# Performance work log

Measured on AMD Instinct MI355X. Metric: run time of the kernel, lower is better.

Reference implementation:

```python
import jax, jax.numpy as jnp
import numpy as np

IN, HID, OUT, HEADS = 64, 128, 256, 4
BL, N, E = 4, 2500, 120000
NT = BL * N  # total flattened nodes = 10000
NEG_SLOPE = 0.2  # PyG GATv2Conv default


def setup_inputs() -> dict:
    key = jax.random.key(0)
    ks = jax.random.split(key, 32)
    inp = {}
    inp["x"] = jax.random.normal(ks[0], (BL, N, IN), jnp.float32)
    inp["edge_index"] = jax.random.randint(ks[1], (2, E), 0, NT, jnp.int32)
    inp["edge_weight"] = jax.random.uniform(ks[2], (E, 1), jnp.float32)
    # layers: (fan_in, out_per_head, heads)
    dims = [(IN, HID, HEADS), (HID * HEADS, HID, HEADS), (HID * HEADS, OUT, 1)]
    i = 3
    for l, (fi, fo, h) in enumerate(dims):
        sc = 1.0 / np.sqrt(fi)
        inp[f"Wl{l}"] = jax.random.normal(ks[i], (fi, h * fo), jnp.float32) * sc
        inp[f"bl{l}"] = jax.random.normal(ks[i + 1], (h * fo,), jnp.float32) * 0.01
        inp[f"Wr{l}"] = jax.random.normal(ks[i + 2], (fi, h * fo), jnp.float32) * sc
        inp[f"br{l}"] = jax.random.normal(ks[i + 3], (h * fo,), jnp.float32) * 0.01
        inp[f"We{l}"] = jax.random.normal(ks[i + 4], (1, h * fo), jnp.float32)
        inp[f"att{l}"] = jax.random.normal(ks[i + 5], (h, fo), jnp.float32) / np.sqrt(fo)
        inp[f"bias{l}"] = jax.random.normal(ks[i + 6], (h * fo,), jnp.float32) * 0.01
        i += 7
    return inp


def _gat_layer(x, src, dst, ew, Wl, bl, Wr, br, We, att, bias):
    # x: (NT, F); ew: (E, 1); att: (H, C)
    H, C = att.shape
    n = x.shape[0]
    xl = (x @ Wl + bl).reshape(n, H, C)          # source transform
    xr = (x @ Wr + br).reshape(n, H, C)          # target transform
    xe = (ew @ We).reshape(-1, H, C)             # edge-attr transform (no bias in PyG lin_edge)
    e = jax.nn.leaky_relu(xl[src] + xr[dst] + xe, negative_slope=NEG_SLOPE)  # (E, H, C)
    logits = jnp.einsum('ehc,hc->eh', e, att)    # (E, H)
    # segment softmax over incoming edges of each destination node
    m = jax.lax.stop_gradient(jax.ops.segment_max(logits, dst, num_segments=n))
    m = jnp.where(jnp.isfinite(m), m, 0.0)
    p = jnp.exp(logits - m[dst])
    s = jax.ops.segment_sum(p, dst, num_segments=n)
    alpha = p / (s[dst] + 1e-16)                 # (E, H)
    msg = xl[src] * alpha[:, :, None]            # (E, H, C)
    out = jax.ops.segment_sum(msg, dst, num_segments=n)  # (NT, H, C)
    return out.reshape(n, H * C) + bias


def reference(x, edge_index, edge_weight,
              Wl0, bl0, Wr0, br0, We0, att0, bias0,
              Wl1, bl1, Wr1, br1, We1, att1, bias1,
              Wl2, bl2, Wr2, br2, We2, att2, bias2):
    bl_, n_, f_ = x.shape
    h = x.reshape(bl_ * n_, f_)
    src, dst = edge_index[0], edge_index[1]
    h = jax.nn.elu(_gat_layer(h, src, dst, edge_weight, Wl0, bl0, Wr0, br0, We0, att0, bias0))
    h = jax.nn.elu(_gat_layer(h, src, dst, edge_weight, Wl1, bl1, Wr1, br1, We1, att1, bias1))
    h = _gat_layer(h, src, dst, edge_weight, Wl2, bl2, Wr2, br2, We2, att2, bias2)
    return h.reshape(bl_, n_, -1)
```

## Files before the change

### kernel.cpp

```cpp
#include <hip/hip_runtime.h>
#include <hip/hip_bf16.h>
#include <math.h>

#define NT    10000
#define NE    120000
#define MP    10240

using h8    = __attribute__((ext_vector_type(8))) _Float16;
using h4    = __attribute__((ext_vector_type(4))) _Float16;
using f32x4 = __attribute__((ext_vector_type(4))) float;

struct Args {
    const float* x;
    const int*   src;
    const int*   dst;
    const float* ew;
    const float* W[6];
    const float* bl[3];
    const float* br[3];
    const float* We[3];
    const float* att[3];
    const float* bias[3];
    _Float16* wt[6];
    _Float16* xf;
    _Float16* xl;  _Float16* xr;
    _Float16* af;
    float* out;
    int* rowptr; int* cntcur; int* csr_src; float* csr_w;
};

__global__ void prep_k(Args a) {
    __shared__ float sf[32 * 33];
    const int mat_cum[7] = {0, 32, 64, 320, 576, 704, 832};
    const int mat_K[6]   = {64, 64, 512, 512, 512, 512};
    const int mat_N[6]   = {512, 512, 512, 512, 256, 256};
    int tid = threadIdx.x;
    int tx = tid & 31, ty = tid >> 5;
    for (int w = blockIdx.x; w < 3411; w += gridDim.x) {
        if (w < 79) {
            int i = w * 256 + tid;
            if (i < 2 * NT) a.cntcur[i] = 0;
        } else if (w < 911) {
            int t = w - 79;
            int mm = 0;
            #pragma unroll
            for (int q = 1; q < 6; ++q) if (t >= mat_cum[q]) mm = q;
            int tt = t - mat_cum[mm];
            int K = mat_K[mm], N = mat_N[mm];
            int tiles_k = K >> 5;
            int tk = tt % tiles_k, tn = tt / tiles_k;
            const float* W = a.W[mm];
            _Float16* T = a.wt[mm];
            int bk = tk * 32, bn = tn * 32;
            __syncthreads();
            #pragma unroll
            for (int i = 0; i < 4; ++i)
                sf[(ty * 4 + i) * 33 + tx] =
                    W[(size_t)(bk + ty * 4 + i) * N + bn + tx];
            __syncthreads();
            #pragma unroll
            for (int i = 0; i < 4; ++i) {
                int nn = ty * 4 + i;
                T[(size_t)(bn + nn) * K + bk + tx] = (_Float16)sf[tx * 33 + nn];
            }
        } else {
            int i = (w - 911) * 256 + tid;
            a.xf[i] = (_Float16)a.x[i];
        }
    }
}

__global__ void hist_k(Args a) {
    for (int e = blockIdx.x * 256 + threadIdx.x; e < NE; e += gridDim.x * 256)
        atomicAdd(&a.cntcur[a.dst[e]], 1);
}

__global__ void scan_k(Args a) {
    __shared__ int si[256];
    int tid = threadIdx.x;
    const int PER = 40;
    int base = tid * PER;
    int s = 0;
    for (int i = 0; i < PER; ++i) {
        int idx = base + i;
        if (idx < NT) s += a.cntcur[idx];
    }
    si[tid] = s;
    __syncthreads();
    for (int off = 1; off < 256; off <<= 1) {
        int v = (tid >= off) ? si[tid - off] : 0;
        __syncthreads();
        si[tid] += v;
        __syncthreads();
    }
    int run = (tid == 0) ? 0 : si[tid - 1];
    for (int i = 0; i < PER; ++i) {
        int idx = base + i;
        if (idx < NT) { a.rowptr[idx] = run; run += a.cntcur[idx]; }
        else if (idx == NT) a.rowptr[idx] = run;
    }
}

__global__ void scatter_k(Args a) {
    int* cursor = a.cntcur + NT;
    for (int e = blockIdx.x * 256 + threadIdx.x; e < NE; e += gridDim.x * 256) {
        int d = a.dst[e];
        int pos = atomicAdd(&cursor[d], 1);
        int idx = a.rowptr[d] + pos;
        a.csr_src[idx] = a.src[e];
        a.csr_w[idx]  = a.ew[e];
    }
}

__global__ __launch_bounds__(256, 4) void gemm_k(
    const _Float16* __restrict__ A,
    const _Float16* __restrict__ WlT, const _Float16* __restrict__ WrT,
    const float* __restrict__ biasl, const float* __restrict__ biasr,
    _Float16* __restrict__ outl, _Float16* __restrict__ outr,
    int M, int N, int K)
{
    __shared__ __align__(16) _Float16 sm[2 * 8192];
    _Float16* sA = sm;
    _Float16* sB = sm + 8192;

    int tid = threadIdx.x;
    int wave = tid >> 6, lane = tid & 63;
    int job = blockIdx.x;

    int xcd = job & 7;
    int kk  = job >> 3;
    int r   = kk % 10;
    int byy = kk / 10;
    int bm  = (xcd * 10 + r) * 128;

    int nby = N >> 7;
    bool isR = byy >= nby;
    int bnn = (isR ? byy - nby : byy) << 7;
    const _Float16* Bh = isR ? WrT : WlT;
    const float* bias  = isR ? biasr : biasl;
    _Float16* out      = isR ? outr : outl;

    int lr15 = lane & 15;
    int lk8  = (lane >> 4) * 8;
    int fq = lane >> 4;
    int fc = lane & 15;
    int wm = (wave & 1) << 6;
    int wn = (wave >> 1) << 6;

    f32x4 acc[4][4] = {};

    for (int k0 = 0; k0 < K; k0 += 64) {
        __syncthreads();
        #pragma unroll
        for (int q = 0; q < 8; ++q) {
            int p = wave * 8 + q;
            int bufi = p >> 4;
            int c = p & 15;
            int sub = c >> 3, rg = c & 7;
            const _Float16* g = (bufi == 0) ? A : Bh;
            int rowbase = (bufi == 0) ? bm : bnn;
            _Float16* sb = sm + bufi * 8192 + c * 512;
            const _Float16* gp = g + (size_t)(rowbase + rg * 16 + lr15) * K
                                   + k0 + sub * 32 + lk8;
            __builtin_amdgcn_global_load_lds(
                (const __attribute__((address_space(1))) void*)gp,
                (__attribute__((address_space(3))) void*)sb,
                16, 0, 0);
        }
        __syncthreads();

        #pragma unroll
        for (int sub = 0; sub < 2; ++sub) {
            h8 af[4];
            #pragma unroll
            for (int i = 0; i < 4; ++i) {
                int c = sub * 8 + (wave & 1) * 4 + i;
                af[i] = *(const h8*)(sA + c * 512 + lane * 8);
            }
            #pragma unroll
            for (int j = 0; j < 4; ++j) {
                int c = sub * 8 + (wave >> 1) * 4 + j;
                h8 bf = *(const h8*)(sB + c * 512 + lane * 8);
                #pragma unroll
                for (int i = 0; i < 4; ++i)
                    acc[i][j] = __builtin_amdgcn_mfma_f32_16x16x32_f16(af[i], bf, acc[i][j], 0, 0, 0);
            }
        }
    }

    #pragma unroll
    for (int j = 0; j < 4; ++j) {
        int col = bnn + wn + j * 16 + fc;
        float bv = bias[col];
        #pragma unroll
        for (int i = 0; i < 4; ++i) {
            int row0 = bm + wm + i * 16 + fq * 4;
            #pragma unroll
            for (int reg = 0; reg < 4; ++reg) {
                int row = row0 + reg;
                if (row < M)
                    out[(size_t)row * N + col] = (_Float16)(acc[i][j][reg] + bv);
            }
        }
    }
}

template<int C, int H, bool DO_ELU, bool FP16OUT>
__global__ __launch_bounds__(256) void edge_k(
    const _Float16* __restrict__ xl, const _Float16* __restrict__ xr,
    const int* __restrict__ rowptr, const int* __restrict__ csr_src,
    const float* __restrict__ csr_w,
    const float* __restrict__ We, const float* __restrict__ att,
    const float* __restrict__ bias,
    float* __restrict__ outf, _Float16* __restrict__ outh)
{
    constexpr int CHT = C * H;
    constexpr int VPT = CHT / 64;
    constexpr int G   = 64 / H;

    int node = (blockIdx.x * 256 + threadIdx.x) >> 6;
    int lane = threadIdx.x & 63;
    if (node >= NT) return;
    int c0 = lane * VPT;
    size_t nbase = (size_t)node * CHT + c0;

    float xr_reg[VPT], we_reg[VPT], att_reg[VPT], bias_reg[VPT];
    {
        _Float16 t[VPT];
        if (VPT == 8) *(h8*)t = *(const h8*)(xr + nbase);
        else          *(h4*)t = *(const h4*)(xr + nbase);
        #pragma unroll
        for (int v = 0; v < VPT; ++v) xr_reg[v] = (float)t[v];
    }
    #pragma unroll
    for (int v = 0; v < VPT; v += 4) {
        *(float4*)(we_reg + v)   = *(const float4*)(We + c0 + v);
        *(float4*)(att_reg + v)  = *(const float4*)(att + c0 + v);
        *(float4*)(bias_reg + v) = *(const float4*)(bias + c0 + v);
    }

    int rs = rowptr[node];
    int re = rowptr[node + 1];

    float m = -INFINITY, ssum = 0.f;
    float av[VPT];
    #pragma unroll
    for (int v = 0; v < VPT; ++v) av[v] = 0.f;

    for (int base = rs; base < re; base += 64) {
        int cn = re - base;
        if (cn > 64) cn = 64;
        int le = base + lane;
        int cl = (le < re) ? le : (re - 1);
        int   sidx = csr_src[cl];
        float swt  = csr_w[cl];

        _Float16 r0[VPT], r1[VPT], r2[VPT];
        auto ld = [&](int j, _Float16* dst) {
            int s = __shfl(sidx, j, 64);
            const _Float16* p = xl + (size_t)s * CHT + c0;
            if (VPT == 8) *(h8*)dst = *(const h8*)p;
            else          *(h4*)dst = *(const h4*)p;
        };
        auto step = [&](const _Float16* rc, int j) {
            float w = __shfl(swt, j, 64);
            float xlv[VPT];
            #pragma unroll
            for (int v = 0; v < VPT; ++v) xlv[v] = (float)rc[v];
            float part = 0.f;
            #pragma unroll
            for (int v = 0; v < VPT; ++v) {
                float t = xlv[v] + xr_reg[v] + w * we_reg[v];
                t = fmaxf(t, 0.f) + 0.2f * fminf(t, 0.f);
                part += t * att_reg[v];
            }
            #pragma unroll
            for (int off = G / 2; off > 0; off >>= 1)
                part += __shfl_xor(part, off, 64);
            float newm = fmaxf(m, part);
            float fac = __expf(m - newm);
            float p = __expf(part - newm);
            ssum = ssum * fac + p;
            #pragma unroll
            for (int v = 0; v < VPT; ++v) av[v] = av[v] * fac + p * xlv[v];
            m = newm;
        };

        ld(0, r0);
        if (cn > 1) ld(1, r1);
        if (cn > 2) ld(2, r2);

        int j = 0;
        while (j < cn) {
            step(r0, j);
            if (j + 3 < cn) ld(j + 3, r0);
            if (++j >= cn) break;
            step(r1, j);
            if (j + 3 < cn) ld(j + 3, r1);
            if (++j >= cn) break;
            step(r2, j);
            if (j + 3 < cn) ld(j + 3, r2);
            ++j;
        }
    }

    float inv = 1.f / (ssum + 1e-16f);
    #pragma unroll
    for (int v = 0; v < VPT; ++v) {
        float o = av[v] * inv + bias_reg[v];
        if (DO_ELU) o = (o > 0.f) ? o : (__expf(o) - 1.f);
        if (FP16OUT) outh[nbase + v] = (_Float16)o;
        else         outf[nbase + v] = o;
    }
}

extern "C" void kernel_launch(void* const* d_in, const int* in_sizes, int n_in,
                              void* d_out, int out_size, void* d_ws, size_t ws_size,
                              hipStream_t stream) {
    Args a;
    a.x   = (const float*)d_in[0];
    const int* ei = (const int*)d_in[1];
    a.src = ei;
    a.dst = ei + NE;
    a.ew  = (const float*)d_in[2];
    for (int l = 0; l < 3; ++l) {
        int base = 3 + 7 * l;
        a.W[2 * l]     = (const float*)d_in[base + 0];
        a.bl[l]        = (const float*)d_in[base + 1];
        a.W[2 * l + 1] = (const float*)d_in[base + 2];
        a.br[l]        = (const float*)d_in[base + 3];
        a.We[l]        = (const float*)d_in[base + 4];
        a.att[l]       = (const float*)d_in[base + 5];
        a.bias[l]      = (const float*)d_in[base + 6];
    }

    size_t off = 0;
    auto alloc = [&](size_t bytes) -> void* {
        void* p = (char*)d_ws + off;
        off += (bytes + 255) & ~(size_t)255;
        return p;
    };
    a.xl   = (_Float16*)alloc((size_t)MP * 512 * 2);
    a.xr   = (_Float16*)alloc((size_t)MP * 512 * 2);
    a.af   = (_Float16*)alloc((size_t)MP * 512 * 2);
    a.xf   = (_Float16*)alloc((size_t)MP * 64 * 2);
    const int KD[3] = {64, 512, 512};
    const int ND[3] = {512, 512, 256};
    for (int l = 0; l < 3; ++l) {
        a.wt[2 * l]     = (_Float16*)alloc((size_t)KD[l] * ND[l] * 2);
        a.wt[2 * l + 1] = (_Float16*)alloc((size_t)KD[l] * ND[l] * 2);
    }
    a.rowptr  = (int*)alloc((size_t)(NT + 1) * 4);
    a.cntcur  = (int*)alloc((size_t)2 * NT * 4);
    a.csr_src = (int*)alloc((size_t)NE * 4);
    a.csr_w   = (float*)alloc((size_t)NE * 4);
    a.out     = (float*)d_out;

    prep_k<<<640, 256, 0, stream>>>(a);
    hist_k<<<469, 256, 0, stream>>>(a);
    scan_k<<<1, 256, 0, stream>>>(a);
    scatter_k<<<469, 256, 0, stream>>>(a);

    gemm_k<<<640, 256, 0, stream>>>(a.xf, a.wt[0], a.wt[1],
                                    a.bl[0], a.br[0], a.xl, a.xr,
                                    NT, 512, 64);
    edge_k<128, 4, true, true><<<2500, 256, 0, stream>>>(
        a.xl, a.xr, a.rowptr, a.csr_src, a.csr_w,
        a.We[0], a.att[0], a.bias[0], nullptr, a.af);

    gemm_k<<<640, 256, 0, stream>>>(a.af, a.wt[2], a.wt[3],
                                    a.bl[1], a.br[1], a.xl, a.xr,
                                    NT, 512, 512);
    edge_k<128, 4, true, true><<<2500, 256, 0, stream>>>(
        a.xl, a.xr, a.rowptr, a.csr_src, a.csr_w,
        a.We[1], a.att[1], a.bias[1], nullptr, a.af);

    gemm_k<<<320, 256, 0, stream>>>(a.af, a.wt[4], a.wt[5],
                                    a.bl[2], a.br[2], a.xl, a.xr,
                                    NT, 256, 512);
    edge_k<256, 1, false, false><<<2500, 256, 0, stream>>>(
        a.xl, a.xr, a.rowptr, a.csr_src, a.csr_w,
        a.We[2], a.att[2], a.bias[2], a.out, nullptr);
}
```

Measured before the change: 300.6 us.

## Fuse prep, histogram, scan, scatter and first GEMM into one cooperative kernel

Merges the preprocessing kernels (weight transpose, counter clear, histogram, scan, CSR scatter) and the layer-0 GEMM into a single cooperative launch separated by grid syncs. The single-block scan runs concurrently with most layer-0 GEMM tiles, and the scatter overlaps the last GEMM tile. This removes several kernel launch gaps and idle time around the serial scan. The cost is grid-wide barriers, and a fallback to separate launches is kept if the cooperative launch fails.

```diff
diff --git a/kernel.cpp b/kernel.cpp
--- a/kernel.cpp
+++ b/kernel.cpp
@@ -1,6 +1,9 @@
 #include <hip/hip_runtime.h>
+#include <hip/hip_cooperative_groups.h>
 #include <hip/hip_bf16.h>
 #include <math.h>
+
+namespace cg = cooperative_groups;
 
 #define NT    10000
 #define NE    120000
@@ -29,14 +32,14 @@
     int* rowptr; int* cntcur; int* csr_src; float* csr_w;
 };
 
-__global__ void prep_k(Args a) {
-    __shared__ float sf[32 * 33];
+__device__ __forceinline__ void prep_phase(const Args& a, int b0, int nb,
+                                           float* sf) {
     const int mat_cum[7] = {0, 32, 64, 320, 576, 704, 832};
     const int mat_K[6]   = {64, 64, 512, 512, 512, 512};
     const int mat_N[6]   = {512, 512, 512, 512, 256, 256};
     int tid = threadIdx.x;
     int tx = tid & 31, ty = tid >> 5;
-    for (int w = blockIdx.x; w < 3411; w += gridDim.x) {
+    for (int w = b0; w < 3411; w += nb) {
         if (w < 79) {
             int i = w * 256 + tid;
             if (i < 2 * NT) a.cntcur[i] = 0;
@@ -70,13 +73,12 @@
     }
 }
 
-__global__ void hist_k(Args a) {
-    for (int e = blockIdx.x * 256 + threadIdx.x; e < NE; e += gridDim.x * 256)
+__device__ __forceinline__ void hist_phase(const Args& a, int b0, int nb) {
+    for (int e = b0 * 256 + (int)threadIdx.x; e < NE; e += nb * 256)
         atomicAdd(&a.cntcur[a.dst[e]], 1);
 }
 
-__global__ void scan_k(Args a) {
-    __shared__ int si[256];
+__device__ __forceinline__ void scan_phase(const Args& a, int* si) {
     int tid = threadIdx.x;
     const int PER = 40;
     int base = tid * PER;
@@ -101,9 +103,9 @@
     }
 }
 
-__global__ void scatter_k(Args a) {
+__device__ __forceinline__ void scatter_phase(const Args& a, int b0, int nb) {
     int* cursor = a.cntcur + NT;
-    for (int e = blockIdx.x * 256 + threadIdx.x; e < NE; e += gridDim.x * 256) {
+    for (int e = b0 * 256 + (int)threadIdx.x; e < NE; e += nb * 256) {
         int d = a.dst[e];
         int pos = atomicAdd(&cursor[d], 1);
         int idx = a.rowptr[d] + pos;
@@ -112,34 +114,18 @@
     }
 }
 
-__global__ __launch_bounds__(256, 4) void gemm_k(
+__device__ __forceinline__ void gemm_jobs(
     const _Float16* __restrict__ A,
     const _Float16* __restrict__ WlT, const _Float16* __restrict__ WrT,
     const float* __restrict__ biasl, const float* __restrict__ biasr,
     _Float16* __restrict__ outl, _Float16* __restrict__ outr,
-    int M, int N, int K)
+    int M, int N, int K, int njobs, int job0, int jstep, _Float16* sm)
 {
-    __shared__ __align__(16) _Float16 sm[2 * 8192];
     _Float16* sA = sm;
     _Float16* sB = sm + 8192;
 
     int tid = threadIdx.x;
     int wave = tid >> 6, lane = tid & 63;
-    int job = blockIdx.x;
-
-    int xcd = job & 7;
-    int kk  = job >> 3;
-    int r   = kk % 10;
-    int byy = kk / 10;
-    int bm  = (xcd * 10 + r) * 128;
-
-    int nby = N >> 7;
-    bool isR = byy >= nby;
-    int bnn = (isR ? byy - nby : byy) << 7;
-    const _Float16* Bh = isR ? WrT : WlT;
-    const float* bias  = isR ? biasr : biasl;
-    _Float16* out      = isR ? outr : outl;
-
     int lr15 = lane & 15;
     int lk8  = (lane >> 4) * 8;
     int fq = lane >> 4;
@@ -147,62 +133,119 @@
     int wm = (wave & 1) << 6;
     int wn = (wave >> 1) << 6;
 
-    f32x4 acc[4][4] = {};
-
-    for (int k0 = 0; k0 < K; k0 += 64) {
+    for (int job = job0; job < njobs; job += jstep) {
+        int xcd = job & 7;
+        int kk  = job >> 3;
+        int r   = kk % 10;
+        int byy = kk / 10;
+        int bm  = (xcd * 10 + r) * 128;
+
+        int nby = N >> 7;
+        bool isR = byy >= nby;
+        int bnn = (isR ? byy - nby : byy) << 7;
+        const _Float16* Bh = isR ? WrT : WlT;
+        const float* bias  = isR ? biasr : biasl;
+        _Float16* out      = isR ? outr : outl;
+
+        f32x4 acc[4][4] = {};
+
+        for (int k0 = 0; k0 < K; k0 += 64) {
+            __syncthreads();
+            #pragma unroll
+            for (int q = 0; q < 8; ++q) {
+                int p = wave * 8 + q;
+                int bufi = p >> 4;
+                int c = p & 15;
+                int sub = c >> 3, rg = c & 7;
+                const _Float16* g = (bufi == 0) ? A : Bh;
+                int rowbase = (bufi == 0) ? bm : bnn;
+                _Float16* sb = sm + bufi * 8192 + c * 512;
+                const _Float16* gp = g + (size_t)(rowbase + rg * 16 + lr15) * K
+                                       + k0 + sub * 32 + lk8;
+                __builtin_amdgcn_global_load_lds(
+                    (const __attribute__((address_space(1))) void*)gp,
+                    (__attribute__((address_space(3))) void*)sb,
+                    16, 0, 0);
+            }
+            __syncthreads();
+
+            #pragma unroll
+            for (int sub = 0; sub < 2; ++sub) {
+                h8 af[4];
+                #pragma unroll
+                for (int i = 0; i < 4; ++i) {
+                    int c = sub * 8 + (wave & 1) * 4 + i;
+                    af[i] = *(const h8*)(sA + c * 512 + lane * 8);
+                }
+                #pragma unroll
+                for (int j = 0; j < 4; ++j) {
+                    int c = sub * 8 + (wave >> 1) * 4 + j;
+                    h8 bf = *(const h8*)(sB + c * 512 + lane * 8);
+                    #pragma unroll
+                    for (int i = 0; i < 4; ++i)
+                        acc[i][j] = __builtin_amdgcn_mfma_f32_16x16x32_f16(af[i], bf, acc[i][j], 0, 0, 0);
+                }
+            }
+        }
+
         __syncthreads();
         #pragma unroll
-        for (int q = 0; q < 8; ++q) {
-            int p = wave * 8 + q;
-            int bufi = p >> 4;
-            int c = p & 15;
-            int sub = c >> 3, rg = c & 7;
-            const _Float16* g = (bufi == 0) ? A : Bh;
-            int rowbase = (bufi == 0) ? bm : bnn;
-            _Float16* sb = sm + bufi * 8192 + c * 512;
-            const _Float16* gp = g + (size_t)(rowbase + rg * 16 + lr15) * K
-                                   + k0 + sub * 32 + lk8;
-            __builtin_amdgcn_global_load_lds(
-                (const __attribute__((address_space(1))) void*)gp,
-                (__attribute__((address_space(3))) void*)sb,
-                16, 0, 0);
-        }
-        __syncthreads();
-
-        #pragma unroll
-        for (int sub = 0; sub < 2; ++sub) {
-            h8 af[4];
+        for (int j = 0; j < 4; ++j) {
+            int col = bnn + wn + j * 16 + fc;
+            float bv = bias[col];
             #pragma unroll
             for (int i = 0; i < 4; ++i) {
-                int c = sub * 8 + (wave & 1) * 4 + i;
-                af[i] = *(const h8*)(sA + c * 512 + lane * 8);
-            }
-            #pragma unroll
-            for (int j = 0; j < 4; ++j) {
-                int c = sub * 8 + (wave >> 1) * 4 + j;
-                h8 bf = *(const h8*)(sB + c * 512 + lane * 8);
+                int row0 = bm + wm + i * 16 + fq * 4;
                 #pragma unroll
-                for (int i = 0; i < 4; ++i)
-                    acc[i][j] = __builtin_amdgcn_mfma_f32_16x16x32_f16(af[i], bf, acc[i][j], 0, 0, 0);
+                for (int reg = 0; reg < 4; ++reg) {
+                    int row = row0 + reg;
+                    if (row < M)
+                        out[(size_t)row * N + col] = (_Float16)(acc[i][j][reg] + bv);
+                }
             }
         }
     }
-
-    #pragma unroll
-    for (int j = 0; j < 4; ++j) {
-        int col = bnn + wn + j * 16 + fc;
-        float bv = bias[col];
-        #pragma unroll
-        for (int i = 0; i < 4; ++i) {
-            int row0 = bm + wm + i * 16 + fq * 4;
-            #pragma unroll
-            for (int reg = 0; reg < 4; ++reg) {
-                int row = row0 + reg;
-                if (row < M)
-                    out[(size_t)row * N + col] = (_Float16)(acc[i][j][reg] + bv);
-            }
-        }
-    }
+}
+
+__global__ __launch_bounds__(256, 4) void head_k(Args a) {
+    cg::grid_group grid = cg::this_grid();
+    __shared__ __align__(16) _Float16 sm[2 * 8192];
+    int b = blockIdx.x, G = gridDim.x;
+
+    prep_phase(a, b, G, (float*)sm);
+    grid.sync();
+
+    hist_phase(a, b, G);
+    grid.sync();
+
+    if (b == 0) scan_phase(a, (int*)sm);
+    else gemm_jobs(a.xf, a.wt[0], a.wt[1], a.bl[0], a.br[0],
+                   a.xl, a.xr, NT, 512, 64, 639, b - 1, G - 1, sm);
+    grid.sync();
+
+    if (b == 0) gemm_jobs(a.xf, a.wt[0], a.wt[1], a.bl[0], a.br[0],
+                          a.xl, a.xr, NT, 512, 64, 640, 639, 1, sm);
+    else scatter_phase(a, b - 1, G - 1);
+}
+
+__global__ void prep_k(Args a) {
+    __shared__ float sf[32 * 33];
+    prep_phase(a, blockIdx.x, gridDim.x, sf);
+}
+__global__ void hist_k(Args a) { hist_phase(a, blockIdx.x, gridDim.x); }
+__global__ void scan_k(Args a) {
+    __shared__ int si[256];
+    scan_phase(a, si);
+}
+__global__ void scatter_k(Args a) { scatter_phase(a, blockIdx.x, gridDim.x); }
+
+__global__ __launch_bounds__(256, 4) void gemm_k(
+    const _Float16* A, const _Float16* WlT, const _Float16* WrT,
+    const float* bl, const float* br,
+    _Float16* ol, _Float16* orr, int M, int N, int K, int njobs) {
+    __shared__ __align__(16) _Float16 sm[2 * 8192];
+    gemm_jobs(A, WlT, WrT, bl, br, ol, orr, M, N, K, njobs,
+              blockIdx.x, gridDim.x, sm);
 }
 
 template<int C, int H, bool DO_ELU, bool FP16OUT>
@@ -356,28 +399,39 @@
     a.csr_w   = (float*)alloc((size_t)NE * 4);
     a.out     = (float*)d_out;
 
-    prep_k<<<640, 256, 0, stream>>>(a);
-    hist_k<<<469, 256, 0, stream>>>(a);
-    scan_k<<<1, 256, 0, stream>>>(a);
-    scatter_k<<<469, 256, 0, stream>>>(a);
-
-    gemm_k<<<640, 256, 0, stream>>>(a.xf, a.wt[0], a.wt[1],
-                                    a.bl[0], a.br[0], a.xl, a.xr,
-                                    NT, 512, 64);
+    void* params[] = { (void*)&a };
+    bool ok = false;
+    const int grids[2] = {640, 512};
+    for (int gi = 0; gi < 2 && !ok; ++gi) {
+        hipError_t err = hipLaunchCooperativeKernel(
+            (const void*)head_k, dim3(grids[gi]), dim3(256), params, 0, stream);
+        if (err == hipSuccess) ok = true;
+        else (void)hipGetLastError();
+    }
+    if (!ok) {
+        prep_k<<<640, 256, 0, stream>>>(a);
+        hist_k<<<469, 256, 0, stream>>>(a);
+        scan_k<<<1, 256, 0, stream>>>(a);
+        scatter_k<<<469, 256, 0, stream>>>(a);
+        gemm_k<<<640, 256, 0, stream>>>(a.xf, a.wt[0], a.wt[1],
+                                        a.bl[0], a.br[0], a.xl, a.xr,
+                                        NT, 512, 64, 640);
+    }
+
     edge_k<128, 4, true, true><<<2500, 256, 0, stream>>>(
         a.xl, a.xr, a.rowptr, a.csr_src, a.csr_w,
         a.We[0], a.att[0], a.bias[0], nullptr, a.af);
 
     gemm_k<<<640, 256, 0, stream>>>(a.af, a.wt[2], a.wt[3],
                                     a.bl[1], a.br[1], a.xl, a.xr,
-                                    NT, 512, 512);
+                                    NT, 512, 512, 640);
     edge_k<128, 4, true, true><<<2500, 256, 0, stream>>>(
         a.xl, a.xr, a.rowptr, a.csr_src, a.csr_w,
         a.We[1], a.att[1], a.bias[1], nullptr, a.af);
 
     gemm_k<<<320, 256, 0, stream>>>(a.af, a.wt[4], a.wt[5],
                                     a.bl[2], a.br[2], a.xl, a.xr,
-                                    NT, 256, 512);
+                                    NT, 256, 512, 320);
     edge_k<256, 1, false, false><<<2500, 256, 0, stream>>>(
         a.xl, a.xr, a.rowptr, a.csr_src, a.csr_w,
         a.We[2], a.att[2], a.bias[2], a.out, nullptr);
```

Result: slower. 542.3 us (+80.4%).

## Fuse setup kernels: merge histogram into prep, overlap CSR scatter with layer-0 GEMM

Applied to the files above, without the earlier changes.

Replaces the cntcur zeroing with a memset and folds the dst histogram into the weight/input prep kernel. The CSR scatter and the first-layer GEMM now run as block-disjoint parts of one launch. The scan uses 1024 threads instead of 256. The aim is fewer kernel launches and serial gaps in graph preprocessing, with the scatter work hidden under the GEMM. Dependencies still hold because the GEMM does not use the CSR arrays.

```diff
diff --git a/kernel.cpp b/kernel.cpp
--- a/kernel.cpp
+++ b/kernel.cpp
@@ -29,19 +29,109 @@
     int* rowptr; int* cntcur; int* csr_src; float* csr_w;
 };
 
-__global__ void prep_k(Args a) {
+__device__ __forceinline__ void gemm_jobs(
+    const _Float16* __restrict__ A,
+    const _Float16* __restrict__ WlT, const _Float16* __restrict__ WrT,
+    const float* __restrict__ biasl, const float* __restrict__ biasr,
+    _Float16* __restrict__ outl, _Float16* __restrict__ outr,
+    int M, int N, int K, int njobs, int job0, int jstep, _Float16* sm)
+{
+    _Float16* sA = sm;
+    _Float16* sB = sm + 8192;
+
+    int tid = threadIdx.x;
+    int wave = tid >> 6, lane = tid & 63;
+    int lr15 = lane & 15;
+    int lk8  = (lane >> 4) * 8;
+    int fq = lane >> 4;
+    int fc = lane & 15;
+    int wm = (wave & 1) << 6;
+    int wn = (wave >> 1) << 6;
+
+    for (int job = job0; job < njobs; job += jstep) {
+        int xcd = job & 7;
+        int kk  = job >> 3;
+        int r   = kk % 10;
+        int byy = kk / 10;
+        int bm  = (xcd * 10 + r) * 128;
+
+        int nby = N >> 7;
+        bool isR = byy >= nby;
+        int bnn = (isR ? byy - nby : byy) << 7;
+        const _Float16* Bh = isR ? WrT : WlT;
+        const float* bias  = isR ? biasr : biasl;
+        _Float16* out      = isR ? outr : outl;
+
+        f32x4 acc[4][4] = {};
+
+        for (int k0 = 0; k0 < K; k0 += 64) {
+            __syncthreads();
+            #pragma unroll
+            for (int q = 0; q < 8; ++q) {
+                int p = wave * 8 + q;
+                int bufi = p >> 4;
+                int c = p & 15;
+                int sub = c >> 3, rg = c & 7;
+                const _Float16* g = (bufi == 0) ? A : Bh;
+                int rowbase = (bufi == 0) ? bm : bnn;
+                _Float16* sb = sm + bufi * 8192 + c * 512;
+                const _Float16* gp = g + (size_t)(rowbase + rg * 16 + lr15) * K
+                                       + k0 + sub * 32 + lk8;
+                __builtin_amdgcn_global_load_lds(
+                    (const __attribute__((address_space(1))) void*)gp,
+                    (__attribute__((address_space(3))) void*)sb,
+                    16, 0, 0);
+            }
+            __syncthreads();
+
+            #pragma unroll
+            for (int sub = 0; sub < 2; ++sub) {
+                h8 af[4];
+                #pragma unroll
+                for (int i = 0; i < 4; ++i) {
+                    int c = sub * 8 + (wave & 1) * 4 + i;
+                    af[i] = *(const h8*)(sA + c * 512 + lane * 8);
+                }
+                #pragma unroll
+                for (int j = 0; j < 4; ++j) {
+                    int c = sub * 8 + (wave >> 1) * 4 + j;
+                    h8 bf = *(const h8*)(sB + c * 512 + lane * 8);
+                    #pragma unroll
+                    for (int i = 0; i < 4; ++i)
+                        acc[i][j] = __builtin_amdgcn_mfma_f32_16x16x32_f16(af[i], bf, acc[i][j], 0, 0, 0);
+                }
+            }
+        }
+
+        __syncthreads();
+        #pragma unroll
+        for (int j = 0; j < 4; ++j) {
+            int col = bnn + wn + j * 16 + fc;
+            float bv = bias[col];
+            #pragma unroll
+            for (int i = 0; i < 4; ++i) {
+                int row0 = bm + wm + i * 16 + fq * 4;
+                #pragma unroll
+                for (int reg = 0; reg < 4; ++reg) {
+                    int row = row0 + reg;
+                    if (row < M)
+                        out[(size_t)row * N + col] = (_Float16)(acc[i][j][reg] + bv);
+                }
+            }
+        }
+    }
+}
+
+__global__ void preph_k(Args a) {
     __shared__ float sf[32 * 33];
     const int mat_cum[7] = {0, 32, 64, 320, 576, 704, 832};
     const int mat_K[6]   = {64, 64, 512, 512, 512, 512};
     const int mat_N[6]   = {512, 512, 512, 512, 256, 256};
     int tid = threadIdx.x;
     int tx = tid & 31, ty = tid >> 5;
-    for (int w = blockIdx.x; w < 3411; w += gridDim.x) {
-        if (w < 79) {
-            int i = w * 256 + tid;
-            if (i < 2 * NT) a.cntcur[i] = 0;
-        } else if (w < 911) {
-            int t = w - 79;
+    for (int w = blockIdx.x; w < 3332; w += gridDim.x) {
+        if (w < 832) {
+            int t = w;
             int mm = 0;
             #pragma unroll
             for (int q = 1; q < 6; ++q) if (t >= mat_cum[q]) mm = q;
@@ -64,21 +154,18 @@
                 T[(size_t)(bn + nn) * K + bk + tx] = (_Float16)sf[tx * 33 + nn];
             }
         } else {
-            int i = (w - 911) * 256 + tid;
+            int i = (w - 832) * 256 + tid;
             a.xf[i] = (_Float16)a.x[i];
         }
     }
-}
-
-__global__ void hist_k(Args a) {
-    for (int e = blockIdx.x * 256 + threadIdx.x; e < NE; e += gridDim.x * 256)
+    for (int e = blockIdx.x * 256 + tid; e < NE; e += gridDim.x * 256)
         atomicAdd(&a.cntcur[a.dst[e]], 1);
 }
 
-__global__ void scan_k(Args a) {
-    __shared__ int si[256];
+__global__ __launch_bounds__(1024) void scan_k(Args a) {
+    __shared__ int si[1024];
     int tid = threadIdx.x;
-    const int PER = 40;
+    const int PER = 10;
     int base = tid * PER;
     int s = 0;
     for (int i = 0; i < PER; ++i) {
@@ -87,7 +174,7 @@
     }
     si[tid] = s;
     __syncthreads();
-    for (int off = 1; off < 256; off <<= 1) {
+    for (int off = 1; off < 1024; off <<= 1) {
         int v = (tid >= off) ? si[tid - off] : 0;
         __syncthreads();
         si[tid] += v;
@@ -101,108 +188,31 @@
     }
 }
 
-__global__ void scatter_k(Args a) {
-    int* cursor = a.cntcur + NT;
-    for (int e = blockIdx.x * 256 + threadIdx.x; e < NE; e += gridDim.x * 256) {
-        int d = a.dst[e];
-        int pos = atomicAdd(&cursor[d], 1);
-        int idx = a.rowptr[d] + pos;
-        a.csr_src[idx] = a.src[e];
-        a.csr_w[idx]  = a.ew[e];
+__global__ __launch_bounds__(256, 4) void scatgemm_k(Args a) {
+    __shared__ __align__(16) _Float16 sm[2 * 8192];
+    int b = blockIdx.x;
+    if (b < 160) {
+        int* cursor = a.cntcur + NT;
+        for (int e = b * 256 + (int)threadIdx.x; e < NE; e += 160 * 256) {
+            int d = a.dst[e];
+            int pos = atomicAdd(&cursor[d], 1);
+            int idx = a.rowptr[d] + pos;
+            a.csr_src[idx] = a.src[e];
+            a.csr_w[idx]  = a.ew[e];
+        }
+    } else {
+        gemm_jobs(a.xf, a.wt[0], a.wt[1], a.bl[0], a.br[0],
+                  a.xl, a.xr, NT, 512, 64, 640, b - 160, 640, sm);
     }
 }
 
 __global__ __launch_bounds__(256, 4) void gemm_k(
-    const _Float16* __restrict__ A,
-    const _Float16* __restrict__ WlT, const _Float16* __restrict__ WrT,
-    const float* __restrict__ biasl, const float* __restrict__ biasr,
-    _Float16* __restrict__ outl, _Float16* __restrict__ outr,
-    int M, int N, int K)
-{
+    const _Float16* A, const _Float16* WlT, const _Float16* WrT,
+    const float* bl, const float* br,
+    _Float16* ol, _Float16* orr, int M, int N, int K, int njobs) {
     __shared__ __align__(16) _Float16 sm[2 * 8192];
-    _Float16* sA = sm;
-    _Float16* sB = sm + 8192;
-
-    int tid = threadIdx.x;
-    int wave = tid >> 6, lane = tid & 63;
-    int job = blockIdx.x;
-
-    int xcd = job & 7;
-    int kk  = job >> 3;
-    int r   = kk % 10;
-    int byy = kk / 10;
-    int bm  = (xcd * 10 + r) * 128;
-
-    int nby = N >> 7;
-    bool isR = byy >= nby;
-    int bnn = (isR ? byy - nby : byy) << 7;
-    const _Float16* Bh = isR ? WrT : WlT;
-    const float* bias  = isR ? biasr : biasl;
-    _Float16* out      = isR ? outr : outl;
-
-    int lr15 = lane & 15;
-    int lk8  = (lane >> 4) * 8;
-    int fq = lane >> 4;
-    int fc = lane & 15;
-    int wm = (wave & 1) << 6;
-    int wn = (wave >> 1) << 6;
-
-    f32x4 acc[4][4] = {};
-
-    for (int k0 = 0; k0 < K; k0 += 64) {
-        __syncthreads();
-        #pragma unroll
-        for (int q = 0; q < 8; ++q) {
-            int p = wave * 8 + q;
-            int bufi = p >> 4;
-            int c = p & 15;
-            int sub = c >> 3, rg = c & 7;
-            const _Float16* g = (bufi == 0) ? A : Bh;
-            int rowbase = (bufi == 0) ? bm : bnn;
-            _Float16* sb = sm + bufi * 8192 + c * 512;
-            const _Float16* gp = g + (size_t)(rowbase + rg * 16 + lr15) * K
-                                   + k0 + sub * 32 + lk8;
-            __builtin_amdgcn_global_load_lds(
-                (const __attribute__((address_space(1))) void*)gp,
-                (__attribute__((address_space(3))) void*)sb,
-                16, 0, 0);
-        }
-        __syncthreads();
-
-        #pragma unroll
-        for (int sub = 0; sub < 2; ++sub) {
-            h8 af[4];
-            #pragma unroll
-            for (int i = 0; i < 4; ++i) {
-                int c = sub * 8 + (wave & 1) * 4 + i;
-                af[i] = *(const h8*)(sA + c * 512 + lane * 8);
-            }
-            #pragma unroll
-            for (int j = 0; j < 4; ++j) {
-                int c = sub * 8 + (wave >> 1) * 4 + j;
-                h8 bf = *(const h8*)(sB + c * 512 + lane * 8);
-                #pragma unroll
-                for (int i = 0; i < 4; ++i)
-                    acc[i][j] = __builtin_amdgcn_mfma_f32_16x16x32_f16(af[i], bf, acc[i][j], 0, 0, 0);
-            }
-        }
-    }
-
-    #pragma unroll
-    for (int j = 0; j < 4; ++j) {
-        int col = bnn + wn + j * 16 + fc;
-        float bv = bias[col];
-        #pragma unroll
-        for (int i = 0; i < 4; ++i) {
-            int row0 = bm + wm + i * 16 + fq * 4;
-            #pragma unroll
-            for (int reg = 0; reg < 4; ++reg) {
-                int row = row0 + reg;
-                if (row < M)
-                    out[(size_t)row * N + col] = (_Float16)(acc[i][j][reg] + bv);
-            }
-        }
-    }
+    gemm_jobs(A, WlT, WrT, bl, br, ol, orr, M, N, K, njobs,
+              blockIdx.x, gridDim.x, sm);
 }
 
 template<int C, int H, bool DO_ELU, bool FP16OUT>
@@ -356,28 +366,25 @@
     a.csr_w   = (float*)alloc((size_t)NE * 4);
     a.out     = (float*)d_out;
 
-    prep_k<<<640, 256, 0, stream>>>(a);
-    hist_k<<<469, 256, 0, stream>>>(a);
-    scan_k<<<1, 256, 0, stream>>>(a);
-    scatter_k<<<469, 256, 0, stream>>>(a);
-
-    gemm_k<<<640, 256, 0, stream>>>(a.xf, a.wt[0], a.wt[1],
-                                    a.bl[0], a.br[0], a.xl, a.xr,
-                                    NT, 512, 64);
+    hipMemsetAsync(a.cntcur, 0, (size_t)2 * NT * 4, stream);
+    preph_k<<<640, 256, 0, stream>>>(a);
+    scan_k<<<1, 1024, 0, stream>>>(a);
+    scatgemm_k<<<800, 256, 0, stream>>>(a);
+
     edge_k<128, 4, true, true><<<2500, 256, 0, stream>>>(
         a.xl, a.xr, a.rowptr, a.csr_src, a.csr_w,
         a.We[0], a.att[0], a.bias[0], nullptr, a.af);
 
     gemm_k<<<640, 256, 0, stream>>>(a.af, a.wt[2], a.wt[3],
                                     a.bl[1], a.br[1], a.xl, a.xr,
-                                    NT, 512, 512);
+                                    NT, 512, 512, 640);
     edge_k<128, 4, true, true><<<2500, 256, 0, stream>>>(
         a.xl, a.xr, a.rowptr, a.csr_src, a.csr_w,
         a.We[1], a.att[1], a.bias[1], nullptr, a.af);
 
     gemm_k<<<320, 256, 0, stream>>>(a.af, a.wt[4], a.wt[5],
                                     a.bl[2], a.br[2], a.xl, a.xr,
-                                    NT, 256, 512);
+                                    NT, 256, 512, 320);
     edge_k<256, 1, false, false><<<2500, 256, 0, stream>>>(
         a.xl, a.xr, a.rowptr, a.csr_src, a.csr_w,
         a.We[2], a.att[2], a.bias[2], a.out, nullptr);
```

New measurement: 285.8 us. -4.9%, faster.
